# Kernel tuning notes

Measured on AMD Instinct MI355X. Metric: run time of the kernel, lower is better.

Reference implementation:

```python
import jax, jax.numpy as jnp
import numpy as np

V_SIZE = jnp.array([0.1, 0.1, 0.2], dtype=jnp.float32)
PC_MIN = jnp.array([0.0, -40.0, -3.0], dtype=jnp.float32)
# normalizer = [vx, vy, vz, vx^2+vy^2+vz^2]
NORMALIZER = jnp.array([0.1, 0.1, 0.2, 0.1**2 + 0.1**2 + 0.2**2], dtype=jnp.float32)
BN_EPS = 1e-5


def setup_inputs() -> dict:
    key = jax.random.key(0)
    ks = jax.random.split(key, 8)
    M, N, NS, C = 100000, 131072, 16, 64
    v_indices = jax.random.randint(ks[0], (M, 4), 0, 40, dtype=jnp.int32)
    v_features = jax.random.normal(ks[1], (M, C), dtype=jnp.float32)
    p_coords = jax.random.uniform(ks[2], (N, 4), dtype=jnp.float32) * 4.0  # bs,x,y,z (bs col unused)
    p_features = jax.random.normal(ks[3], (N, C), dtype=jnp.float32)
    p_map = jax.random.randint(ks[4], (N, NS), 0, M, dtype=jnp.int32)  # global voxel indices
    p_mask = (jax.random.uniform(ks[5], (N, NS)) > 0.25).astype(jnp.float32)
    W = jax.random.normal(ks[6], (C, C), dtype=jnp.float32) * 0.05  # Linear weight [out,in]
    gamma = jnp.ones((C,), dtype=jnp.float32)
    beta = jnp.zeros((C,), dtype=jnp.float32)
    bn_mean = jnp.zeros((C,), dtype=jnp.float32)
    bn_var = jnp.ones((C,), dtype=jnp.float32)
    return {"v_indices": v_indices, "v_features": v_features, "p_coords": p_coords,
            "p_features": p_features, "p_map": p_map, "p_mask": p_mask,
            "W": W, "gamma": gamma, "beta": beta, "bn_mean": bn_mean, "bn_var": bn_var}


def reference(v_indices, v_features, p_coords, p_features, p_map, p_mask,
              W, gamma, beta, bn_mean, bn_var):
    # voxel center coords from integer indices: [M,3]
    v_xyz = (v_indices[:, jnp.array([3, 2, 1])].astype(jnp.float32) + 0.5) * V_SIZE + PC_MIN
    # gather: [N, ns, 3] and [N, ns, C]
    g_coords = v_xyz[p_map]
    g_feats = v_features[p_map]
    # geometric kernel ('xyz'): relative coords + squared distance, normalized
    centers = p_coords[:, 1:4]                      # [N,3]
    rel = g_coords - centers[:, None, :]            # [N,ns,3]
    dist = jnp.sum(rel * rel, axis=2, keepdims=True)  # [N,ns,1]
    geo = jnp.concatenate([rel, dist], axis=2) / NORMALIZER  # [N,ns,4]
    # FC (no bias) + BatchNorm1d (inference stats) + ReLU
    h = jnp.einsum('nsc,oc->nso', g_feats, W)
    h = (h - bn_mean) * (gamma / jnp.sqrt(bn_var + BN_EPS)) + beta
    h = jax.nn.relu(h)                              # [N,ns,C]
    C = h.shape[2]
    geo_rep = jnp.tile(geo, (1, 1, C // 4))         # [N,ns,C]
    weighted = h * geo_rep * p_mask[:, :, None]
    denom = jnp.clip(jnp.sum(p_mask, axis=1, keepdims=True), 1.0)
    pooled = jnp.sum(weighted, axis=1) / denom      # [N,C]
    return p_features + pooled
```

## Files before the change

### kernel.cpp

```cpp
#include <hip/hip_runtime.h>

#define CH 64

typedef _Float16 half8  __attribute__((ext_vector_type(8)));
typedef _Float16 half2v __attribute__((ext_vector_type(2)));
typedef float    f32x4  __attribute__((ext_vector_type(4)));

__device__ __forceinline__ half8 cvt_half8(float4 a, float4 b) {
    half8 h;
    h[0] = (_Float16)a.x; h[1] = (_Float16)a.y; h[2] = (_Float16)a.z; h[3] = (_Float16)a.w;
    h[4] = (_Float16)b.x; h[5] = (_Float16)b.y; h[6] = (_Float16)b.z; h[7] = (_Float16)b.w;
    return h;
}

__global__ __launch_bounds__(256) void voxel_mlp_mfma(
    const int4*   __restrict__ vi4,
    const float4* __restrict__ vf4,
    const float4* __restrict__ Wf4,
    const float*  __restrict__ gamma,
    const float*  __restrict__ beta,
    const float*  __restrict__ bn_mean,
    const float*  __restrict__ bn_var,
    unsigned*     __restrict__ Hvp,
    float4*       __restrict__ Vxyz,
    int M)
{
    const int t     = threadIdx.x;
    const int lane  = t & 63;
    const int wv    = t >> 6;
    const int row16 = lane & 15;
    const int kgrp  = lane >> 4;
    const int blockRow = blockIdx.x * 64;

    if (t < 64) {
        int r = blockRow + t;
        if (r < M) {
            int4 vi = vi4[r];
            float4 vx;
            vx.x = ((float)vi.w + 0.5f) * 0.1f;
            vx.y = ((float)vi.z + 0.5f) * 0.1f - 40.0f;
            vx.z = ((float)vi.y + 0.5f) * 0.2f - 3.0f;
            vx.w = 0.0f;
            Vxyz[r] = vx;
        }
    }

    half8 bfrag[4][2];
    #pragma unroll
    for (int ot = 0; ot < 4; ++ot) {
        int o = ot * 16 + row16;
        #pragma unroll
        for (int ck = 0; ck < 2; ++ck) {
            int c4 = ck * 8 + kgrp * 2;
            bfrag[ot][ck] = cvt_half8(Wf4[o * 16 + c4], Wf4[o * 16 + c4 + 1]);
        }
    }

    const int rbase = blockRow + wv * 16;
    int rc = rbase + row16; if (rc > M - 1) rc = M - 1;
    half8 afrag[2];
    #pragma unroll
    for (int ck = 0; ck < 2; ++ck) {
        int c4 = ck * 8 + kgrp * 2;
        afrag[ck] = cvt_half8(vf4[rc * 16 + c4], vf4[rc * 16 + c4 + 1]);
    }

    f32x4 acc[4] = {{0.f,0.f,0.f,0.f},{0.f,0.f,0.f,0.f},{0.f,0.f,0.f,0.f},{0.f,0.f,0.f,0.f}};
    #pragma unroll
    for (int ot = 0; ot < 4; ++ot) {
        acc[ot] = __builtin_amdgcn_mfma_f32_16x16x32_f16(afrag[0], bfrag[ot][0], acc[ot], 0, 0, 0);
        acc[ot] = __builtin_amdgcn_mfma_f32_16x16x32_f16(afrag[1], bfrag[ot][1], acc[ot], 0, 0, 0);
    }

    float sc[4], sh[4];
    #pragma unroll
    for (int ot = 0; ot < 4; ++ot) {
        int o = ot * 16 + row16;
        float s = gamma[o] * rsqrtf(bn_var[o] + 1e-5f);
        sc[ot] = s;
        sh[ot] = beta[o] - bn_mean[o] * s;
    }

    #pragma unroll
    for (int reg = 0; reg < 4; ++reg) {
        int row = rbase + kgrp * 4 + reg;
        if (row < M) {
            #pragma unroll
            for (int ot = 0; ot < 2; ++ot) {
                float v0 = fmaxf(fmaf(acc[ot][reg],     sc[ot],     sh[ot]),     0.f);
                float v1 = fmaxf(fmaf(acc[ot + 2][reg], sc[ot + 2], sh[ot + 2]), 0.f);
                half2v p; p[0] = (_Float16)v0; p[1] = (_Float16)v1;
                *reinterpret_cast<half2v*>(&Hvp[row * 32 + ot * 16 + row16]) = p;
            }
        }
    }
}

__device__ __forceinline__ void pool_point_compute(
    int n, int g, int k, int q0,
    float wsel, float mk, const uint2* h01,
    float2 pf, float* __restrict__ out, bool doStore)
{
    float den = mk;
    den += __shfl_xor(den, 4);
    den += __shfl_xor(den, 8);
    den += __shfl_xor(den, 16);
    den += __shfl_xor(den, 32);
    den = fmaxf(den, 1.0f);

    float acc0 = 0.f, acc1 = 0.f, acc2 = 0.f, acc3 = 0.f;
    #pragma unroll
    for (int i = 0; i < 4; ++i) {
        const int sl = (g << 4) + (i << 2) + q0;
        float wlo = __shfl(wsel, sl);
        float whi = __shfl(wsel, sl + 1);
        half2v a = __builtin_bit_cast(half2v, h01[i].x);
        half2v b = __builtin_bit_cast(half2v, h01[i].y);
        acc0 = fmaf((float)a[0], wlo, acc0);
        acc1 = fmaf((float)b[0], whi, acc1);
        acc2 = fmaf((float)a[1], wlo, acc2);
        acc3 = fmaf((float)b[1], whi, acc3);
    }
    acc0 += __shfl_xor(acc0, 16); acc0 += __shfl_xor(acc0, 32);
    acc1 += __shfl_xor(acc1, 16); acc1 += __shfl_xor(acc1, 32);
    acc2 += __shfl_xor(acc2, 16); acc2 += __shfl_xor(acc2, 32);
    acc3 += __shfl_xor(acc3, 16); acc3 += __shfl_xor(acc3, 32);

    if (doStore) {
        float r = 1.0f / den;
        float2 o;
        if (g == 0) { o.x = fmaf(acc0, r, pf.x); o.y = fmaf(acc1, r, pf.y); }
        else        { o.x = fmaf(acc2, r, pf.x); o.y = fmaf(acc3, r, pf.y); }
        *reinterpret_cast<float2*>(out + n * 64 + g * 32 + k * 2) = o;
    }
}

__global__ __launch_bounds__(256) void pool_kernel(
    const float*  __restrict__ p_coords,
    const float*  __restrict__ p_features,
    const int*    __restrict__ p_map,
    const float*  __restrict__ p_mask,
    const char*   __restrict__ Hvp,
    const float4* __restrict__ Vxyz,
    float* __restrict__ out,
    int N)
{
    const int lane = threadIdx.x & 63;
    const int wv   = threadIdx.x >> 6;
    int n0 = __builtin_amdgcn_readfirstlane(((int)blockIdx.x * 4 + wv) * 2);
    if (n0 >= N) return;
    int n1 = n0 + 1;
    const bool has1 = (n1 < N);
    if (!has1) n1 = n0;

    const int g  = lane >> 4;
    const int k  = lane & 15;
    const int q0 = (lane & 1) * 2;
    const int sp = lane >> 2;
    const int j  = lane & 3;

    const int4 m4a = ((const int4*)(p_map + n0 * 16))[g];
    const int4 m4b = ((const int4*)(p_map + n1 * 16))[g];
    const unsigned co = (unsigned)k * 8u;

    uint2 ha[4], hb[4];
    ha[0] = *(const uint2*)(Hvp + ((unsigned)m4a.x * 128u + co));
    ha[1] = *(const uint2*)(Hvp + ((unsigned)m4a.y * 128u + co));
    ha[2] = *(const uint2*)(Hvp + ((unsigned)m4a.z * 128u + co));
    ha[3] = *(const uint2*)(Hvp + ((unsigned)m4a.w * 128u + co));
    hb[0] = *(const uint2*)(Hvp + ((unsigned)m4b.x * 128u + co));
    hb[1] = *(const uint2*)(Hvp + ((unsigned)m4b.y * 128u + co));
    hb[2] = *(const uint2*)(Hvp + ((unsigned)m4b.z * 128u + co));
    hb[3] = *(const uint2*)(Hvp + ((unsigned)m4b.w * 128u + co));

    const int   mia = p_map [n0 * 16 + sp];
    const int   mib = p_map [n1 * 16 + sp];
    const float mka = p_mask[n0 * 16 + sp];
    const float mkb = p_mask[n1 * 16 + sp];
    const float4 va = Vxyz[mia];
    const float4 vb = Vxyz[mib];

    float2 pfa = make_float2(0.f, 0.f), pfb = make_float2(0.f, 0.f);
    if (g < 2) {
        pfa = *(const float2*)(p_features + n0 * 64 + g * 32 + k * 2);
        pfb = *(const float2*)(p_features + n1 * 64 + g * 32 + k * 2);
    }

    {
        const float cx = p_coords[n0 * 4 + 1];
        const float cy = p_coords[n0 * 4 + 2];
        const float cz = p_coords[n0 * 4 + 3];
        float rx = va.x - cx, ry = va.y - cy, rz = va.z - cz;
        float d  = fmaf(rx, rx, fmaf(ry, ry, rz * rz));
        float lo = (j & 1) ? ry * 10.0f : rx * 10.0f;
        float hi = (j & 1) ? d * (1.0f / 0.06f) : rz * 5.0f;
        float wsel = ((j & 2) ? hi : lo) * mka;
        pool_point_compute(n0, g, k, q0, wsel, mka, ha, pfa, out, g < 2);
    }
    {
        const float cx = p_coords[n1 * 4 + 1];
        const float cy = p_coords[n1 * 4 + 2];
        const float cz = p_coords[n1 * 4 + 3];
        float rx = vb.x - cx, ry = vb.y - cy, rz = vb.z - cz;
        float d  = fmaf(rx, rx, fmaf(ry, ry, rz * rz));
        float lo = (j & 1) ? ry * 10.0f : rx * 10.0f;
        float hi = (j & 1) ? d * (1.0f / 0.06f) : rz * 5.0f;
        float wsel = ((j & 2) ? hi : lo) * mkb;
        pool_point_compute(n1, g, k, q0, wsel, mkb, hb, pfb, out, (g < 2) && has1);
    }
}

extern "C" void kernel_launch(void* const* d_in, const int* in_sizes, int n_in,
                              void* d_out, int out_size, void* d_ws, size_t ws_size,
                              hipStream_t stream) {
    const int*   v_indices  = (const int*)  d_in[0];
    const float* v_features = (const float*)d_in[1];
    const float* p_coords   = (const float*)d_in[2];
    const float* p_features = (const float*)d_in[3];
    const int*   p_map      = (const int*)  d_in[4];
    const float* p_mask     = (const float*)d_in[5];
    const float* W          = (const float*)d_in[6];
    const float* gamma      = (const float*)d_in[7];
    const float* beta       = (const float*)d_in[8];
    const float* bn_mean    = (const float*)d_in[9];
    const float* bn_var     = (const float*)d_in[10];

    const int M = in_sizes[1] / CH;
    const int N = in_sizes[3] / CH;

    unsigned* Hvp  = (unsigned*)d_ws;
    float4*   Vxyz = (float4*)((char*)d_ws + (size_t)M * 128);

    {
        dim3 grid((M + 63) / 64);
        voxel_mlp_mfma<<<grid, 256, 0, stream>>>(
            (const int4*)v_indices, (const float4*)v_features, (const float4*)W,
            gamma, beta, bn_mean, bn_var, Hvp, Vxyz, M);
    }
    {
        dim3 grid((N + 7) / 8);
        pool_kernel<<<grid, 256, 0, stream>>>(
            p_coords, p_features, p_map, p_mask,
            (const char*)Hvp, (const float4*)Vxyz, (float*)d_out, N);
    }
}
```

Before: 76.46 us.

## Skip masked voxel gathers, prepack W to fp16, use packed RTZ converts

The pool kernel now loads the mask as float4 alongside the map and only gathers voxel features for neighbours with a nonzero mask, zero-filling the rest. This cuts random global-memory traffic for the roughly quarter of masked entries. A tiny separate kernel pre-converts W into fp16 MFMA fragment layout, so each voxel block loads ready-made fragments instead of converting them. Conversions use packed round-toward-zero instructions, which slightly changes rounding and adds a launch.

```diff
diff --git a/kernel.cpp b/kernel.cpp
--- a/kernel.cpp
+++ b/kernel.cpp
@@ -4,19 +4,38 @@
 
 typedef _Float16 half8  __attribute__((ext_vector_type(8)));
 typedef _Float16 half2v __attribute__((ext_vector_type(2)));
+typedef __fp16   fp16x2 __attribute__((ext_vector_type(2)));
 typedef float    f32x4  __attribute__((ext_vector_type(4)));
 
-__device__ __forceinline__ half8 cvt_half8(float4 a, float4 b) {
+__device__ __forceinline__ half2v pk(float a, float b) {
+    fp16x2 r = __builtin_amdgcn_cvt_pkrtz(a, b);
+    return __builtin_bit_cast(half2v, r);
+}
+
+__global__ __launch_bounds__(512) void prepack_w(
+    const float4* __restrict__ Wf4,
+    half8* __restrict__ Whp8)
+{
+    const int t = threadIdx.x;
+    const int o    = t & 63;
+    const int grp  = t >> 6;
+    const int kgrp = grp & 3;
+    const int ck   = grp >> 2;
+    const int c4   = ck * 8 + kgrp * 2;
+    float4 a = Wf4[o * 16 + c4];
+    float4 b = Wf4[o * 16 + c4 + 1];
     half8 h;
-    h[0] = (_Float16)a.x; h[1] = (_Float16)a.y; h[2] = (_Float16)a.z; h[3] = (_Float16)a.w;
-    h[4] = (_Float16)b.x; h[5] = (_Float16)b.y; h[6] = (_Float16)b.z; h[7] = (_Float16)b.w;
-    return h;
+    half2v p0 = pk(a.x, a.y), p1 = pk(a.z, a.w);
+    half2v p2 = pk(b.x, b.y), p3 = pk(b.z, b.w);
+    h[0]=p0[0]; h[1]=p0[1]; h[2]=p1[0]; h[3]=p1[1];
+    h[4]=p2[0]; h[5]=p2[1]; h[6]=p3[0]; h[7]=p3[1];
+    Whp8[t] = h;
 }
 
 __global__ __launch_bounds__(256) void voxel_mlp_mfma(
     const int4*   __restrict__ vi4,
     const float4* __restrict__ vf4,
-    const float4* __restrict__ Wf4,
+    const half8*  __restrict__ Whp8,
     const float*  __restrict__ gamma,
     const float*  __restrict__ beta,
     const float*  __restrict__ bn_mean,
@@ -47,13 +66,10 @@
 
     half8 bfrag[4][2];
     #pragma unroll
-    for (int ot = 0; ot < 4; ++ot) {
-        int o = ot * 16 + row16;
+    for (int ck = 0; ck < 2; ++ck) {
         #pragma unroll
-        for (int ck = 0; ck < 2; ++ck) {
-            int c4 = ck * 8 + kgrp * 2;
-            bfrag[ot][ck] = cvt_half8(Wf4[o * 16 + c4], Wf4[o * 16 + c4 + 1]);
-        }
+        for (int ot = 0; ot < 4; ++ot)
+            bfrag[ot][ck] = Whp8[(ck * 4 + kgrp) * 64 + ot * 16 + row16];
     }
 
     const int rbase = blockRow + wv * 16;
@@ -62,7 +78,14 @@
     #pragma unroll
     for (int ck = 0; ck < 2; ++ck) {
         int c4 = ck * 8 + kgrp * 2;
-        afrag[ck] = cvt_half8(vf4[rc * 16 + c4], vf4[rc * 16 + c4 + 1]);
+        float4 a = vf4[rc * 16 + c4];
+        float4 b = vf4[rc * 16 + c4 + 1];
+        half8 h;
+        half2v p0 = pk(a.x, a.y), p1 = pk(a.z, a.w);
+        half2v p2 = pk(b.x, b.y), p3 = pk(b.z, b.w);
+        h[0]=p0[0]; h[1]=p0[1]; h[2]=p1[0]; h[3]=p1[1];
+        h[4]=p2[0]; h[5]=p2[1]; h[6]=p3[0]; h[7]=p3[1];
+        afrag[ck] = h;
     }
 
     f32x4 acc[4] = {{0.f,0.f,0.f,0.f},{0.f,0.f,0.f,0.f},{0.f,0.f,0.f,0.f},{0.f,0.f,0.f,0.f}};
@@ -89,7 +112,7 @@
             for (int ot = 0; ot < 2; ++ot) {
                 float v0 = fmaxf(fmaf(acc[ot][reg],     sc[ot],     sh[ot]),     0.f);
                 float v1 = fmaxf(fmaf(acc[ot + 2][reg], sc[ot + 2], sh[ot + 2]), 0.f);
-                half2v p; p[0] = (_Float16)v0; p[1] = (_Float16)v1;
+                half2v p = pk(v0, v1);
                 *reinterpret_cast<half2v*>(&Hvp[row * 32 + ot * 16 + row16]) = p;
             }
         }
@@ -159,19 +182,23 @@
     const int sp = lane >> 2;
     const int j  = lane & 3;
 
-    const int4 m4a = ((const int4*)(p_map + n0 * 16))[g];
-    const int4 m4b = ((const int4*)(p_map + n1 * 16))[g];
+    const int4   m4a  = ((const int4*)  (p_map  + n0 * 16))[g];
+    const int4   m4b  = ((const int4*)  (p_map  + n1 * 16))[g];
+    const float4 mk4a = ((const float4*)(p_mask + n0 * 16))[g];
+    const float4 mk4b = ((const float4*)(p_mask + n1 * 16))[g];
     const unsigned co = (unsigned)k * 8u;
 
     uint2 ha[4], hb[4];
-    ha[0] = *(const uint2*)(Hvp + ((unsigned)m4a.x * 128u + co));
-    ha[1] = *(const uint2*)(Hvp + ((unsigned)m4a.y * 128u + co));
-    ha[2] = *(const uint2*)(Hvp + ((unsigned)m4a.z * 128u + co));
-    ha[3] = *(const uint2*)(Hvp + ((unsigned)m4a.w * 128u + co));
-    hb[0] = *(const uint2*)(Hvp + ((unsigned)m4b.x * 128u + co));
-    hb[1] = *(const uint2*)(Hvp + ((unsigned)m4b.y * 128u + co));
-    hb[2] = *(const uint2*)(Hvp + ((unsigned)m4b.z * 128u + co));
-    hb[3] = *(const uint2*)(Hvp + ((unsigned)m4b.w * 128u + co));
+    #pragma unroll
+    for (int i = 0; i < 4; ++i) { ha[i] = make_uint2(0u,0u); hb[i] = make_uint2(0u,0u); }
+    if (mk4a.x != 0.f) ha[0] = *(const uint2*)(Hvp + ((unsigned)m4a.x * 128u + co));
+    if (mk4a.y != 0.f) ha[1] = *(const uint2*)(Hvp + ((unsigned)m4a.y * 128u + co));
+    if (mk4a.z != 0.f) ha[2] = *(const uint2*)(Hvp + ((unsigned)m4a.z * 128u + co));
+    if (mk4a.w != 0.f) ha[3] = *(const uint2*)(Hvp + ((unsigned)m4a.w * 128u + co));
+    if (mk4b.x != 0.f) hb[0] = *(const uint2*)(Hvp + ((unsigned)m4b.x * 128u + co));
+    if (mk4b.y != 0.f) hb[1] = *(const uint2*)(Hvp + ((unsigned)m4b.y * 128u + co));
+    if (mk4b.z != 0.f) hb[2] = *(const uint2*)(Hvp + ((unsigned)m4b.z * 128u + co));
+    if (mk4b.w != 0.f) hb[3] = *(const uint2*)(Hvp + ((unsigned)m4b.w * 128u + co));
 
     const int   mia = p_map [n0 * 16 + sp];
     const int   mib = p_map [n1 * 16 + sp];
@@ -230,11 +257,13 @@
 
     unsigned* Hvp  = (unsigned*)d_ws;
     float4*   Vxyz = (float4*)((char*)d_ws + (size_t)M * 128);
-
+    half8*    Whp8 = (half8*)((char*)d_ws + (size_t)M * 144);
+
+    prepack_w<<<1, 512, 0, stream>>>((const float4*)W, Whp8);
     {
         dim3 grid((M + 63) / 64);
         voxel_mlp_mfma<<<grid, 256, 0, stream>>>(
-            (const int4*)v_indices, (const float4*)v_features, (const float4*)W,
+            (const int4*)v_indices, (const float4*)v_features, Whp8,
             gamma, beta, bn_mean, bn_var, Hvp, Vxyz, M);
     }
     {
```

After: 64.62 us. 1.18x faster.
